# Optimization experiments

Hardware: AMD Instinct MI355X
Metric: run time of the kernel (lower is better)

## Reference

```python
import jax, jax.numpy as jnp
import numpy as np

B, T, V, D, L, FFM = 2, 2048, 50257, 1024, 8, 2


def setup_inputs() -> dict:
    key = jax.random.key(0)
    ks = jax.random.split(key, 10)
    s = 0.02
    return {
        "input_ids": jax.random.randint(ks[0], (B, T), 0, V),
        "embed": jax.random.normal(ks[1], (V, D), jnp.float32) * s,
        "norm1_w": jnp.ones((L, D), jnp.float32),
        "norm2_w": jnp.ones((L, D), jnp.float32),
        "a_diag": jax.random.uniform(ks[2], (L, D), jnp.float32, 0.5, 0.99),
        "W_in": jax.random.normal(ks[3], (L, D, D), jnp.float32) * s,
        "b_in": jnp.zeros((L, D), jnp.float32),
        "W_out": jax.random.normal(ks[4], (L, D, D), jnp.float32) * s,
        "ff_w1": jax.random.normal(ks[5], (L, D, FFM * D), jnp.float32) * s,
        "ff_b1": jnp.zeros((L, FFM * D), jnp.float32),
        "ff_w2": jax.random.normal(ks[6], (L, FFM * D, D), jnp.float32) * s,
        "ff_b2": jnp.zeros((L, D), jnp.float32),
        "final_norm_w": jnp.ones((D,), jnp.float32),
        "lm_head_w": jax.random.normal(ks[7], (V, D), jnp.float32) * s,
    }


def rmsnorm(x, w, eps=1e-6):
    return x * jax.lax.rsqrt(jnp.mean(x * x, axis=-1, keepdims=True) + eps) * w


def chaos_core(x, a, Win, bin_, Wout):
    pre = jnp.einsum('btd,de->bte', x, Win) + bin_  # precompute input drive (parallel)

    def step(s, p):
        s = jnp.tanh(a * s + p)
        return s, s

    s0 = jnp.zeros((x.shape[0], x.shape[-1]), x.dtype)
    _, hs = jax.lax.scan(step, s0, jnp.swapaxes(pre, 0, 1))  # (T, B, D)
    hs = jnp.swapaxes(hs, 0, 1)  # (B, T, D)
    return jnp.einsum('btd,de->bte', hs, Wout)


def reference(input_ids, embed, norm1_w, norm2_w, a_diag, W_in, b_in, W_out,
              ff_w1, ff_b1, ff_w2, ff_b2, final_norm_w, lm_head_w):
    x = embed[input_ids]  # (B, T, D)
    for i in range(L):
        # input_norm -> core -> residual
        x = x + chaos_core(rmsnorm(x, norm1_w[i]), a_diag[i], W_in[i], b_in[i], W_out[i])
        # ff_norm -> FeedForward (Linear -> SiLU -> Linear) -> residual
        h = rmsnorm(x, norm2_w[i])
        h = jax.nn.silu(jnp.einsum('btd,df->btf', h, ff_w1[i]) + ff_b1[i])
        x = x + jnp.einsum('btf,fd->btd', h, ff_w2[i]) + ff_b2[i]
    x = rmsnorm(x, final_norm_w)
    return jnp.einsum('btd,vd->btv', x, lm_head_w)  # logits (B, T, V)
```

## Files before the change

### kernel.cpp

```cpp
#include <hip/hip_runtime.h>

typedef unsigned short u16;
typedef __bf16 bf16x8 __attribute__((ext_vector_type(8)));
typedef float f32x4 __attribute__((ext_vector_type(4)));
typedef unsigned short u16x4 __attribute__((ext_vector_type(4)));

__device__ __forceinline__ u16 f2bf(float f) {
  union { float f; unsigned int u; } v; v.f = f;
  return (u16)((v.u + 0x7FFFu + ((v.u >> 16) & 1u)) >> 16);
}

__device__ __forceinline__ void gload16(const void* g, void* l) {
  __builtin_amdgcn_global_load_lds(
      (const __attribute__((address_space(1))) unsigned int*)g,
      (__attribute__((address_space(3))) unsigned int*)l, 16, 0, 0);
}

__global__ __launch_bounds__(256) void prep_all(
    const float* __restrict__ Win, const float* __restrict__ Wout,
    const float* __restrict__ ffw1, const float* __restrict__ ffw2,
    u16* __restrict__ WinT, u16* __restrict__ WoutT,
    u16* __restrict__ f1T, u16* __restrict__ f2T,
    const float* __restrict__ lmw, u16* __restrict__ lmpad,
    const int* __restrict__ ids, const float* __restrict__ embedw,
    float* __restrict__ x) {
  __shared__ float tile[32][33];
  const int bid = blockIdx.x;
  const int tid = threadIdx.x;

  if (bid >= 49152 + 50432) {
    const int row = bid - (49152 + 50432);
    *(float4*)(x + (size_t)row * 1024 + tid * 4) =
        *(const float4*)(embedw + (size_t)ids[row] * 1024 + tid * 4);
    return;
  }
  if (bid >= 49152) {
    const int row = bid - 49152;
    u16x4 o = {0, 0, 0, 0};
    if (row < 50257) {
      float4 v = *(const float4*)(lmw + (size_t)row * 1024 + tid * 4);
      o.x = f2bf(v.x); o.y = f2bf(v.y); o.z = f2bf(v.z); o.w = f2bf(v.w);
    }
    *(u16x4*)(lmpad + (size_t)row * 1024 + tid * 4) = o;
    return;
  }

  const int tk = bid;
  const float* src; u16* dst;
  int R, C, tr, tc;
  if (tk < 8192) {
    const int l = tk >> 10, rem = tk & 1023;
    R = 1024; C = 1024; tr = rem >> 5; tc = rem & 31;
    src = Win + (size_t)l * 1048576; dst = WinT + (size_t)l * 1048576;
  } else if (tk < 16384) {
    const int q = tk - 8192, l = q >> 10, rem = q & 1023;
    R = 1024; C = 1024; tr = rem >> 5; tc = rem & 31;
    src = Wout + (size_t)l * 1048576; dst = WoutT + (size_t)l * 1048576;
  } else if (tk < 32768) {
    const int q = tk - 16384, l = q >> 11, rem = q & 2047;
    R = 1024; C = 2048; tr = rem >> 6; tc = rem & 63;
    src = ffw1 + (size_t)l * 2097152; dst = f1T + (size_t)l * 2097152;
  } else {
    const int q = tk - 32768, l = q >> 11, rem = q & 2047;
    R = 2048; C = 1024; tr = rem >> 5; tc = rem & 31;
    src = ffw2 + (size_t)l * 2097152; dst = f2T + (size_t)l * 2097152;
  }
  const int tx = tid & 31, ty = tid >> 5;
  const int c0 = tc * 32, r0 = tr * 32;
#pragma unroll
  for (int k = 0; k < 32; k += 8)
    tile[ty + k][tx] = src[(size_t)(r0 + ty + k) * C + (c0 + tx)];
  __syncthreads();
#pragma unroll
  for (int k = 0; k < 32; k += 8)
    dst[(size_t)(c0 + ty + k) * R + (r0 + tx)] = f2bf(tile[tx][ty + k]);
}

__global__ void rmsnorm_kernel(const float* __restrict__ x, const float* __restrict__ w,
                               u16* __restrict__ out) {
  const int row = blockIdx.x, tid = threadIdx.x;
  const float* xr = x + (size_t)row * 1024;
  float4 v = *(const float4*)(xr + tid * 4);
  float ss = v.x * v.x + v.y * v.y + v.z * v.z + v.w * v.w;
#pragma unroll
  for (int off = 32; off; off >>= 1) ss += __shfl_xor(ss, off);
  __shared__ float red[4];
  if ((tid & 63) == 0) red[tid >> 6] = ss;
  __syncthreads();
  const float tot = red[0] + red[1] + red[2] + red[3];
  const float r = rsqrtf(tot * (1.0f / 1024.0f) + 1e-6f);
  float4 wv = *(const float4*)(w + tid * 4);
  u16x4 o;
  o.x = f2bf(v.x * r * wv.x); o.y = f2bf(v.y * r * wv.y);
  o.z = f2bf(v.z * r * wv.z); o.w = f2bf(v.w * r * wv.w);
  *(u16x4*)(out + (size_t)row * 1024 + tid * 4) = o;
}

__device__ __forceinline__ void sload(const float* __restrict__ p, int tb,
                                      float A2b, float (&buf)[8]) {
#pragma unroll
  for (int j = 0; j < 8; j++)
    buf[j] = fmaf(p[(size_t)(tb + j) * 1024], 2.8853900817779268f, A2b);
}

__device__ __forceinline__ void scomp(float (&buf)[8], float m2A2, float& r,
                                      u16* __restrict__ o, int tb) {
#pragma unroll
  for (int j = 0; j < 8; j++) {
    float z = fmaf(m2A2, r, buf[j]);
    float e = __builtin_amdgcn_exp2f(z);
    r = __builtin_amdgcn_rcpf(1.0f + e);
    o[(size_t)(tb + j) * 1024] = f2bf(fmaf(-2.0f, r, 1.0f));
  }
}

__global__ __launch_bounds__(256) void scan_kernel(const float* __restrict__ pre,
                                                   const float* __restrict__ a_diag,
                                                   const float* __restrict__ b_in,
                                                   u16* __restrict__ hs) {
  const int T = 2048;
  const int idx = blockIdx.x * 256 + threadIdx.x;
  const int b = idx >> 10, d = idx & 1023;
  const float* p = pre + (size_t)b * T * 1024 + d;
  u16* o = hs + (size_t)b * T * 1024 + d;
  const float A2 = a_diag[d] * 2.8853900817779268f;
  const float A2b = fmaf(2.8853900817779268f, b_in[d], A2);
  const float m2A2 = -2.0f * A2;
  float r = 0.5f;
  float b0[8], b1[8], b2[8], b3[8];
  sload(p, 0, A2b, b0); sload(p, 8, A2b, b1);
  sload(p, 16, A2b, b2); sload(p, 24, A2b, b3);
  for (int t0 = 0; t0 < T; t0 += 32) {
    scomp(b0, m2A2, r, o, t0);
    if (t0 + 32 < T) sload(p, t0 + 32, A2b, b0);
    scomp(b1, m2A2, r, o, t0 + 8);
    if (t0 + 32 < T) sload(p, t0 + 40, A2b, b1);
    scomp(b2, m2A2, r, o, t0 + 16);
    if (t0 + 32 < T) sload(p, t0 + 48, A2b, b2);
    scomp(b3, m2A2, r, o, t0 + 24);
    if (t0 + 32 < T) sload(p, t0 + 56, A2b, b3);
  }
}

template <int EPI>
__global__ __launch_bounds__(256) void gemmL(
    const u16* __restrict__ A, int lda, const u16* __restrict__ Bw, int ldb,
    const float* __restrict__ bias, float* Cf, u16* __restrict__ Cb,
    int ldc, int K) {
  __shared__ char lds[49152];
  const int tid = threadIdx.x;
  const int lane = tid & 63;
  const int wc = tid >> 6;
  const int tm = blockIdx.y * 64, tn = blockIdx.x * 128;
  const int lr = lane & 15;
  const int sb0 = ((lane >> 4) ^ (lane & 7)) << 4;

  const int srow = tid >> 3;
  const int sxs = ((tid & 7) ^ (srow & 7)) << 4;
  const char* pA = (const char*)A + (size_t)(tm + srow) * lda * 2 + sxs;
  const char* pB = (const char*)Bw + (size_t)(tn + srow) * ldb * 2 + sxs;
  const size_t a32 = (size_t)lda * 64;
  const size_t b32 = (size_t)ldb * 64;

#define STGL(kt, bufo)                                \
  {                                                   \
    char* d = lds + (bufo) + tid * 16;                \
    const size_t kb = (size_t)(kt) << 7;              \
    gload16(pA + kb, d);                              \
    gload16(pA + a32 + kb, d + 4096);                 \
    gload16(pB + kb, d + 8192);                       \
    gload16(pB + b32 + kb, d + 12288);                \
    gload16(pB + 2 * b32 + kb, d + 16384);            \
    gload16(pB + 3 * b32 + kb, d + 20480);            \
  }

  f32x4 acc[4][2] = {};
  const int nkt = K >> 6;

  STGL(0, 0);
  int cur = 0;
  for (int kt = 0; kt < nkt; ++kt) {
    if (kt + 1 < nkt) {
      STGL(kt + 1, (cur ^ 1) * 24576);
      asm volatile("s_waitcnt vmcnt(6)" ::: "memory");
    } else {
      asm volatile("s_waitcnt vmcnt(0)" ::: "memory");
    }
    __builtin_amdgcn_s_barrier();
    const char* base = lds + cur * 24576;
    bf16x8 aF[4][2], bF[2][2];
#pragma unroll
    for (int m = 0; m < 4; m++)
#pragma unroll
      for (int ks = 0; ks < 2; ks++)
        aF[m][ks] =
            *(const bf16x8*)(base + (m * 16 + lr) * 128 + (sb0 ^ (ks << 6)));
#pragma unroll
    for (int n = 0; n < 2; n++)
#pragma unroll
      for (int ks = 0; ks < 2; ks++)
        bF[n][ks] = *(const bf16x8*)(base + 8192 +
                                     (wc * 32 + n * 16 + lr) * 128 +
                                     (sb0 ^ (ks << 6)));
#pragma unroll
    for (int ks = 0; ks < 2; ks++)
#pragma unroll
      for (int m = 0; m < 4; m++)
#pragma unroll
        for (int n = 0; n < 2; n++)
          acc[m][n] = __builtin_amdgcn_mfma_f32_16x16x32_bf16(
              aF[m][ks], bF[n][ks], acc[m][n], 0, 0, 0);
    __builtin_amdgcn_s_barrier();
    cur ^= 1;
  }
#undef STGL

  const int crow = tm + ((lane >> 4) << 2);
  const int ccol = tn + wc * 32 + lr;
#pragma unroll
  for (int m = 0; m < 4; m++) {
#pragma unroll
    for (int n = 0; n < 2; n++) {
      const int cg = ccol + n * 16;
      float bb = 0.0f;
      if (EPI == 2 || EPI == 3) bb = bias[cg];
#pragma unroll
      for (int j = 0; j < 4; j++) {
        const size_t off = (size_t)(crow + m * 16 + j) * ldc + cg;
        const float v = acc[m][n][j] + bb;
        if (EPI == 0) {
          Cf[off] = v;
        } else if (EPI == 1) {
          Cf[off] += v;
        } else if (EPI == 2) {
          const float sg = __builtin_amdgcn_rcpf(
              1.0f + __builtin_amdgcn_exp2f(-1.4426950408889634f * v));
          Cb[off] = f2bf(v * sg);
        } else {
          Cf[off] += v;
        }
      }
    }
  }
}

__global__ __launch_bounds__(256) void gemm_lm128(
    const u16* __restrict__ A, const u16* __restrict__ Bw,
    float* __restrict__ C, int Nreal) {
  __shared__ char lds[65536];
  const int tid = threadIdx.x;
  const int lane = tid & 63;
  const int wid = tid >> 6;
  const int wm = wid >> 1, wn = wid & 1;
  const int bid = blockIdx.x;
  const int tm = (((bid & 7) << 2) + ((bid >> 3) & 3)) << 7;
  const int tn = (bid >> 5) << 7;

  const int lr = lane & 15;
  const int sb0 = ((lane >> 4) ^ (lane & 7)) << 4;
  const int sb[2] = {sb0, sb0 ^ 64};

  const int srow = tid >> 3;
  const int sxs = ((tid & 7) ^ (srow & 7)) << 4;
  const char* pA = (const char*)A + ((size_t)(tm + srow) << 11) + sxs;
  const char* pB = (const char*)Bw + ((size_t)(tn + srow) << 11) + sxs;
  const size_t p32 = (size_t)32 << 11;

#define STG128(kt, bufo)                               \
  {                                                    \
    char* d = lds + (bufo) + tid * 16;                 \
    const size_t kb = (size_t)(kt) << 7;               \
    gload16(pA + kb, d);                               \
    gload16(pA + p32 + kb, d + 4096);                  \
    gload16(pA + 2 * p32 + kb, d + 8192);              \
    gload16(pA + 3 * p32 + kb, d + 12288);             \
    gload16(pB + kb, d + 16384);                       \
    gload16(pB + p32 + kb, d + 20480);                 \
    gload16(pB + 2 * p32 + kb, d + 24576);             \
    gload16(pB + 3 * p32 + kb, d + 28672);             \
  }

  const int aB0 = (wm * 64 + lr) * 128;
  const int bB0 = 16384 + (wn * 64 + lr) * 128;

  f32x4 acc[4][4] = {};

  STG128(0, 0);
  int cur = 0;
  for (int kt = 0; kt < 16; ++kt) {
    if (kt + 1 < 16) {
      STG128(kt + 1, (cur ^ 1) * 32768);
      asm volatile("s_waitcnt vmcnt(8)" ::: "memory");
    } else {
      asm volatile("s_waitcnt vmcnt(0)" ::: "memory");
    }
    __builtin_amdgcn_s_barrier();
    const char* base = lds + cur * 32768;
    bf16x8 aF[4][2], bF[4][2];
#pragma unroll
    for (int m = 0; m < 4; m++)
#pragma unroll
      for (int ks = 0; ks < 2; ks++) {
        aF[m][ks] = *(const bf16x8*)(base + aB0 + m * 2048 + sb[ks]);
        bF[m][ks] = *(const bf16x8*)(base + bB0 + m * 2048 + sb[ks]);
      }
    __builtin_amdgcn_s_setprio(1);
#pragma unroll
    for (int ks = 0; ks < 2; ks++)
#pragma unroll
      for (int m = 0; m < 4; m++)
#pragma unroll
        for (int n = 0; n < 4; n++)
          acc[m][n] = __builtin_amdgcn_mfma_f32_16x16x32_bf16(
              aF[m][ks], bF[n][ks], acc[m][n], 0, 0, 0);
    __builtin_amdgcn_s_setprio(0);
    __builtin_amdgcn_s_barrier();
    cur ^= 1;
  }
#undef STG128

  const int crow = tm + wm * 64 + ((lane >> 4) << 2);
  const int ccol = tn + wn * 64 + lr;
#pragma unroll
  for (int m = 0; m < 4; m++) {
#pragma unroll
    for (int n = 0; n < 4; n++) {
      const int cg = ccol + n * 16;
      if (cg < Nreal) {
#pragma unroll
        for (int j = 0; j < 4; j++)
          C[(size_t)(crow + m * 16 + j) * Nreal + cg] = acc[m][n][j];
      }
    }
  }
}

extern "C" void kernel_launch(void* const* d_in, const int* in_sizes, int n_in,
                              void* d_out, int out_size, void* d_ws, size_t ws_size,
                              hipStream_t stream) {
  const int D = 1024, V = 50257, L = 8;
  const int M = 4096;
  const int Vpad = 50432;
  const size_t MD = (size_t)M * D;

  const int* ids = (const int*)d_in[0];
  const float* embedw = (const float*)d_in[1];
  const float* norm1_w = (const float*)d_in[2];
  const float* norm2_w = (const float*)d_in[3];
  const float* a_diag = (const float*)d_in[4];
  const float* W_in = (const float*)d_in[5];
  const float* b_in = (const float*)d_in[6];
  const float* W_out = (const float*)d_in[7];
  const float* ff_w1 = (const float*)d_in[8];
  const float* ff_b1 = (const float*)d_in[9];
  const float* ff_w2 = (const float*)d_in[10];
  const float* ff_b2 = (const float*)d_in[11];
  const float* final_norm_w = (const float*)d_in[12];
  const float* lm_head_w = (const float*)d_in[13];

  char* w = (char*)d_ws;
  float* x = (float*)w;   w += MD * 4;
  u16* h = (u16*)w;       w += MD * 2;
  float* pre = (float*)w; w += MD * 4;
  u16* hs = (u16*)w;      w += MD * 2;
  u16* hff = (u16*)w;     w += MD * 2 * 2;
  u16* WinT = (u16*)w;    w += (size_t)L * D * D * 2;
  u16* WoutT = (u16*)w;   w += (size_t)L * D * D * 2;
  u16* ffw1T = (u16*)w;   w += (size_t)L * 2 * D * D * 2;
  u16* ffw2T = (u16*)w;   w += (size_t)L * 2 * D * D * 2;
  u16* lmpad = (u16*)w;   w += (size_t)Vpad * D * 2;

  prep_all<<<49152 + Vpad + M, 256, 0, stream>>>(
      W_in, W_out, ff_w1, ff_w2, WinT, WoutT, ffw1T, ffw2T,
      lm_head_w, lmpad, ids, embedw, x);

  for (int l = 0; l < L; l++) {
    rmsnorm_kernel<<<M, 256, 0, stream>>>(x, norm1_w + (size_t)l * D, h);
    gemmL<0><<<dim3(8, 64), 256, 0, stream>>>(
        h, D, WinT + (size_t)l * D * D, D, nullptr, pre, nullptr, D, D);
    scan_kernel<<<8, 256, 0, stream>>>(pre, a_diag + (size_t)l * D,
                                       b_in + (size_t)l * D, hs);
    gemmL<1><<<dim3(8, 64), 256, 0, stream>>>(
        hs, D, WoutT + (size_t)l * D * D, D, nullptr, x, nullptr, D, D);
    rmsnorm_kernel<<<M, 256, 0, stream>>>(x, norm2_w + (size_t)l * D, h);
    gemmL<2><<<dim3(16, 64), 256, 0, stream>>>(
        h, D, ffw1T + (size_t)l * 2 * D * D, D, ff_b1 + (size_t)l * 2 * D,
        nullptr, hff, 2 * D, D);
    gemmL<3><<<dim3(8, 64), 256, 0, stream>>>(
        hff, 2 * D, ffw2T + (size_t)l * 2 * D * D, 2 * D,
        ff_b2 + (size_t)l * D, x, nullptr, D, 2 * D);
  }

  rmsnorm_kernel<<<M, 256, 0, stream>>>(x, final_norm_w, h);
  gemm_lm128<<<dim3(32 * 394), 256, 0, stream>>>(h, lmpad, (float*)d_out, V);
}
```

Baseline: 2.779 ms.

## Retile LM-head GEMM to 256x256 tiles with 512 threads and K-step 32

Replaces the 128x128-tile LM-head GEMM with a 256x256 tile computed by 8 waves, each holding a 128x64 accumulator block, and shrinks the K step per stage to 32. The larger tile halves global traffic per output and raises MFMA density per LDS read. The cost is more accumulator registers and twice as many barrier-separated K iterations. It also drops the LDS XOR swizzle, which may bring back bank conflicts on the 64-byte row stride.

```diff
diff --git a/kernel.cpp b/kernel.cpp
--- a/kernel.cpp
+++ b/kernel.cpp
@@ -244,92 +244,85 @@
   }
 }
 
-__global__ __launch_bounds__(256) void gemm_lm128(
+__global__ __launch_bounds__(512, 2) void gemm_lm32(
     const u16* __restrict__ A, const u16* __restrict__ Bw,
     float* __restrict__ C, int Nreal) {
   __shared__ char lds[65536];
   const int tid = threadIdx.x;
   const int lane = tid & 63;
   const int wid = tid >> 6;
-  const int wm = wid >> 1, wn = wid & 1;
+  const int wr = wid >> 2;
+  const int wc = wid & 3;
   const int bid = blockIdx.x;
-  const int tm = (((bid & 7) << 2) + ((bid >> 3) & 3)) << 7;
-  const int tn = (bid >> 5) << 7;
+  const int tm = (((bid & 7) << 1) + ((bid >> 3) & 1)) << 8;
+  const int tn = (bid >> 4) << 8;
+
+  const int srow = tid >> 2;
+  const char* pA = (const char*)A + ((size_t)(tm + srow) << 11) + ((tid & 3) << 4);
+  const char* pB = (const char*)Bw + ((size_t)(tn + srow) << 11) + ((tid & 3) << 4);
+  const size_t r128 = (size_t)128 << 11;
+
+#define STG32(kt, bufo)                         \
+  {                                             \
+    char* d = lds + (bufo) + tid * 16;          \
+    const size_t kb = (size_t)(kt) << 6;        \
+    gload16(pA + kb, d);                        \
+    gload16(pA + r128 + kb, d + 8192);          \
+    gload16(pB + kb, d + 16384);                \
+    gload16(pB + r128 + kb, d + 24576);         \
+  }
 
   const int lr = lane & 15;
-  const int sb0 = ((lane >> 4) ^ (lane & 7)) << 4;
-  const int sb[2] = {sb0, sb0 ^ 64};
-
-  const int srow = tid >> 3;
-  const int sxs = ((tid & 7) ^ (srow & 7)) << 4;
-  const char* pA = (const char*)A + ((size_t)(tm + srow) << 11) + sxs;
-  const char* pB = (const char*)Bw + ((size_t)(tn + srow) << 11) + sxs;
-  const size_t p32 = (size_t)32 << 11;
-
-#define STG128(kt, bufo)                               \
-  {                                                    \
-    char* d = lds + (bufo) + tid * 16;                 \
-    const size_t kb = (size_t)(kt) << 7;               \
-    gload16(pA + kb, d);                               \
-    gload16(pA + p32 + kb, d + 4096);                  \
-    gload16(pA + 2 * p32 + kb, d + 8192);              \
-    gload16(pA + 3 * p32 + kb, d + 12288);             \
-    gload16(pB + kb, d + 16384);                       \
-    gload16(pB + p32 + kb, d + 20480);                 \
-    gload16(pB + 2 * p32 + kb, d + 24576);             \
-    gload16(pB + 3 * p32 + kb, d + 28672);             \
-  }
-
-  const int aB0 = (wm * 64 + lr) * 128;
-  const int bB0 = 16384 + (wn * 64 + lr) * 128;
-
-  f32x4 acc[4][4] = {};
-
-  STG128(0, 0);
+  const int kg = (lane >> 4) << 4;
+  int aOff[8], bOff[4];
+#pragma unroll
+  for (int m = 0; m < 8; m++) aOff[m] = (wr * 128 + m * 16 + lr) * 64 + kg;
+#pragma unroll
+  for (int n = 0; n < 4; n++) bOff[n] = 16384 + (wc * 64 + n * 16 + lr) * 64 + kg;
+
+  f32x4 acc[8][4] = {};
+
+  STG32(0, 0);
   int cur = 0;
-  for (int kt = 0; kt < 16; ++kt) {
-    if (kt + 1 < 16) {
-      STG128(kt + 1, (cur ^ 1) * 32768);
-      asm volatile("s_waitcnt vmcnt(8)" ::: "memory");
+  for (int kt = 0; kt < 32; ++kt) {
+    if (kt + 1 < 32) {
+      STG32(kt + 1, (cur ^ 1) * 32768);
+      asm volatile("s_waitcnt vmcnt(4)" ::: "memory");
     } else {
       asm volatile("s_waitcnt vmcnt(0)" ::: "memory");
     }
     __builtin_amdgcn_s_barrier();
     const char* base = lds + cur * 32768;
-    bf16x8 aF[4][2], bF[4][2];
-#pragma unroll
-    for (int m = 0; m < 4; m++)
-#pragma unroll
-      for (int ks = 0; ks < 2; ks++) {
-        aF[m][ks] = *(const bf16x8*)(base + aB0 + m * 2048 + sb[ks]);
-        bF[m][ks] = *(const bf16x8*)(base + bB0 + m * 2048 + sb[ks]);
-      }
+    bf16x8 aF[8], bF[4];
+#pragma unroll
+    for (int m = 0; m < 8; m++) aF[m] = *(const bf16x8*)(base + aOff[m]);
+#pragma unroll
+    for (int n = 0; n < 4; n++) bF[n] = *(const bf16x8*)(base + bOff[n]);
     __builtin_amdgcn_s_setprio(1);
 #pragma unroll
-    for (int ks = 0; ks < 2; ks++)
-#pragma unroll
-      for (int m = 0; m < 4; m++)
-#pragma unroll
-        for (int n = 0; n < 4; n++)
-          acc[m][n] = __builtin_amdgcn_mfma_f32_16x16x32_bf16(
-              aF[m][ks], bF[n][ks], acc[m][n], 0, 0, 0);
+    for (int m = 0; m < 8; m++)
+#pragma unroll
+      for (int n = 0; n < 4; n++)
+        acc[m][n] = __builtin_amdgcn_mfma_f32_16x16x32_bf16(
+            aF[m], bF[n], acc[m][n], 0, 0, 0);
     __builtin_amdgcn_s_setprio(0);
     __builtin_amdgcn_s_barrier();
     cur ^= 1;
   }
-#undef STG128
-
-  const int crow = tm + wm * 64 + ((lane >> 4) << 2);
-  const int ccol = tn + wn * 64 + lr;
-#pragma unroll
-  for (int m = 0; m < 4; m++) {
+#undef STG32
+
+  const int crow = tm + wr * 128 + ((lane >> 4) << 2);
+  const int ccol = tn + wc * 64 + lr;
+#pragma unroll
+  for (int m = 0; m < 8; m++) {
+    const int r = crow + m * 16;
 #pragma unroll
     for (int n = 0; n < 4; n++) {
       const int cg = ccol + n * 16;
       if (cg < Nreal) {
 #pragma unroll
         for (int j = 0; j < 4; j++)
-          C[(size_t)(crow + m * 16 + j) * Nreal + cg] = acc[m][n][j];
+          C[(size_t)(r + j) * Nreal + cg] = acc[m][n][j];
       }
     }
   }
@@ -392,5 +385,5 @@
   }
 
   rmsnorm_kernel<<<M, 256, 0, stream>>>(x, final_norm_w, h);
-  gemm_lm128<<<dim3(32 * 394), 256, 0, stream>>>(h, lmpad, (float*)d_out, V);
-}
+  gemm_lm32<<<dim3(8 * 394), 512, 0, stream>>>(h, lmpad, (float*)d_out, V);
+}
```

Result: no change. 2.778 ms (-0.1%).
